# Performance work log

Hardware: AMD Instinct MI355X
Metric: run time of the kernel (lower is better)

The kernel has to match this reference:

```python
import jax, jax.numpy as jnp
import numpy as np

N = 262144   # tokens
L = 128      # ldims (per-direction LSTM feature size)
H = 128      # hidden_units
H2 = 128     # hidden2_units
R = 64       # number of relation labels


def setup_inputs() -> dict:
    key = jax.random.key(0)
    ks = jax.random.split(key, 12)
    glorot = lambda k, shape: jax.random.uniform(
        k, shape, jnp.float32, -1.0, 1.0) * np.sqrt(6.0 / (shape[0] + shape[1]))
    return {
        "fwd": jax.random.normal(ks[0], (N, L), jnp.float32),
        "bwd": jax.random.normal(ks[1], (N, L), jnp.float32),
        "gold_heads": jax.random.randint(ks[2], (N - 1,), 0, N),
        "gold_rels": jax.random.randint(ks[3], (N - 1,), 0, R),
        "WFOH": glorot(ks[4], (2 * L, H)),
        "WFOM": glorot(ks[5], (2 * L, H)),
        "rhidBias": glorot(ks[6], (1, H)),
        "rcatBias": glorot(ks[7], (1, 2 * H)),
        "rhid2Layer": glorot(ks[8], (2 * H, H2)),
        "rhid2Bias": glorot(ks[9], (1, H2)),
        "routLayer": glorot(ks[10], (H2, R)),
        "routBias": glorot(ks[11], (1, R)),
    }


def reference(fwd, bwd, gold_heads, gold_rels, WFOH, WFOM, rhidBias,
              rcatBias, rhid2Layer, rhid2Bias, routLayer, routBias):
    E = gold_heads.shape[0]
    mods = jnp.arange(E) + 1                       # modifiers are tokens 1..N-1
    # per-edge concat(head fwd-state, modifier bwd-state): (E, 2L)
    cat = jnp.concatenate([fwd[gold_heads], bwd[mods]], axis=-1)
    headfov = cat @ WFOH                           # (E, H)
    modfov = cat @ WFOM                            # (E, H)
    # hidden2_units > 0 branch of __evaluateLabel
    h = jnp.tanh(jnp.concatenate([headfov, modfov], axis=-1) + rcatBias)  # (E, 2H)
    h2 = jnp.tanh(h @ rhid2Layer + rhid2Bias)      # (E, H2)
    scores = h2 @ routLayer + routBias             # (E, R)
    # hinge: best wrong label vs gold label, loss only if margin violated
    gold_s = jnp.take_along_axis(scores, gold_rels[:, None], axis=1)[:, 0]
    masked = jnp.where(jnp.arange(R)[None, :] == gold_rels[:, None], -jnp.inf, scores)
    wrong_idx = jnp.argmax(masked, axis=1)
    wrong_s = jnp.take_along_axis(scores, wrong_idx[:, None], axis=1)[:, 0]
    lerrs = jnp.where(gold_s < wrong_s + 1.0, wrong_s - gold_s, 0.0)  # (E,)
    return lerrs
```

## Files before the change

### kernel.cpp

```cpp
#include <hip/hip_runtime.h>
#include <hip/hip_bf16.h>

typedef __bf16 bf16x8 __attribute__((ext_vector_type(8)));
typedef float  f32x4  __attribute__((ext_vector_type(4)));

#define MFMA16 __builtin_amdgcn_mfma_f32_16x16x32_bf16

__device__ __forceinline__ float fast_tanh(float x) {
    float e = __builtin_amdgcn_exp2f(x * 2.8853900817779268f);
    return 1.0f - 2.0f * __builtin_amdgcn_rcpf(e + 1.0f);
}

__device__ __forceinline__ unsigned short f2bf(float f) {
    unsigned u = __builtin_bit_cast(unsigned, f);
    u += 0x7fffu + ((u >> 16) & 1u);
    return (unsigned short)(u >> 16);
}

__global__ __launch_bounds__(512, 2) void rel_kernel(
    const float* __restrict__ fwd, const float* __restrict__ bwd,
    const int* __restrict__ gold_heads, const int* __restrict__ gold_rels,
    const float* __restrict__ WFOH, const float* __restrict__ WFOM,
    const float* __restrict__ rcatBias, const float* __restrict__ rhid2Layer,
    const float* __restrict__ rhid2Bias, const float* __restrict__ routLayer,
    const float* __restrict__ routBias, float* __restrict__ out,
    int E, int NT)
{
    __shared__ __align__(16) char sh_cat[32 * 512];
    __shared__ __align__(16) char sh_h  [32 * 512];
    __shared__ __align__(16) char sh_h2 [32 * 256];
    __shared__ __align__(16) char sh_sc [32 * 256];
    __shared__ float sh_catf[256];
    __shared__ float sh_hf[256];
    __shared__ float sh_h2f[128];
    __shared__ float sh_scf[64];
    __shared__ int sh_nfix;
    __shared__ int sh_fixlist[8];

    const int tid   = threadIdx.x;
    const int w     = tid >> 6;
    const int lane  = tid & 63;
    const int row16 = lane & 15;
    const int g     = lane >> 4;
    const int xm    = (row16 & 7) << 4;

    bf16x8 w1f[2][8];
    #pragma unroll
    for (int nbl = 0; nbl < 2; ++nbl) {
        int n = 32 * w + 16 * nbl + row16;
        const float* Wsrc = (n < 128) ? WFOH : WFOM;
        int col = (n < 128) ? n : (n - 128);
        #pragma unroll
        for (int kk = 0; kk < 8; ++kk) {
            bf16x8 f;
            #pragma unroll
            for (int j = 0; j < 8; ++j) {
                int k = 32 * kk + 8 * g + j;
                f[j] = (__bf16)Wsrc[k * 128 + col];
            }
            w1f[nbl][kk] = f;
        }
    }
    bf16x8 w2f[8];
    {
        int n2 = 16 * w + row16;
        #pragma unroll
        for (int kk = 0; kk < 8; ++kk) {
            bf16x8 f;
            #pragma unroll
            for (int j = 0; j < 8; ++j) {
                int k = 32 * kk + 8 * g + j;
                f[j] = (__bf16)rhid2Layer[k * 128 + n2];
            }
            w2f[kk] = f;
        }
    }
    const int mb3 = w >> 2, nb3 = w & 3;
    bf16x8 w3f[4];
    {
        int n3 = 16 * nb3 + row16;
        #pragma unroll
        for (int kk = 0; kk < 4; ++kk) {
            bf16x8 f;
            #pragma unroll
            for (int j = 0; j < 8; ++j) {
                int k = 32 * kk + 8 * g + j;
                f[j] = (__bf16)routLayer[k * 64 + n3];
            }
            w3f[kk] = f;
        }
    }
    const float rcb0 = rcatBias[32 * w + row16];
    const float rcb1 = rcatBias[32 * w + 16 + row16];
    const float r2b  = rhid2Bias[16 * w + row16];
    const float rob  = routBias[16 * nb3 + row16];

    const int sr = tid >> 4;
    const int sq = tid & 15;
    const int xr_st = (sr & 7) << 4;

    float4 pf[4];
    auto load_tile = [&](int t) {
        int e = t * 32 + sr;
        if (e < E) {
            const float* src;
            if (sq < 8) {
                int head = gold_heads[e];
                src = fwd + (size_t)head * 128 + sq * 16;
            } else {
                src = bwd + (size_t)(e + 1) * 128 + (sq - 8) * 16;
            }
            const float4* p4 = reinterpret_cast<const float4*>(src);
            #pragma unroll
            for (int c = 0; c < 4; ++c) pf[c] = p4[c];
        } else {
            #pragma unroll
            for (int c = 0; c < 4; ++c) pf[c] = make_float4(0.f, 0.f, 0.f, 0.f);
        }
    };

    int tile0 = blockIdx.x;
    if (tile0 < NT) load_tile(tile0);

    for (int tile = tile0; tile < NT; tile += gridDim.x) {
        const int e0 = tile * 32;

        #pragma unroll
        for (int c = 0; c < 4; ++c) {
            uint2 pk;
            pk.x = (unsigned)f2bf(pf[c].x) | ((unsigned)f2bf(pf[c].y) << 16);
            pk.y = (unsigned)f2bf(pf[c].z) | ((unsigned)f2bf(pf[c].w) << 16);
            int off = sr * 512 + ((32 * sq + 8 * c) ^ xr_st);
            *(uint2*)(sh_cat + off) = pk;
        }
        __syncthreads();

        if (tile + gridDim.x < NT) load_tile(tile + gridDim.x);

        f32x4 acc1[2][2];
        #pragma unroll
        for (int a = 0; a < 2; ++a)
            #pragma unroll
            for (int b = 0; b < 2; ++b) acc1[a][b] = (f32x4){0.f, 0.f, 0.f, 0.f};
        #pragma unroll
        for (int kk = 0; kk < 8; ++kk) {
            int ko = (64 * kk + 16 * g) ^ xm;
            bf16x8 a0 = *(const bf16x8*)(sh_cat + row16 * 512 + ko);
            bf16x8 a1 = *(const bf16x8*)(sh_cat + (16 + row16) * 512 + ko);
            acc1[0][0] = MFMA16(a0, w1f[0][kk], acc1[0][0], 0, 0, 0);
            acc1[1][0] = MFMA16(a1, w1f[0][kk], acc1[1][0], 0, 0, 0);
            acc1[0][1] = MFMA16(a0, w1f[1][kk], acc1[0][1], 0, 0, 0);
            acc1[1][1] = MFMA16(a1, w1f[1][kk], acc1[1][1], 0, 0, 0);
        }
        #pragma unroll
        for (int mb = 0; mb < 2; ++mb)
            #pragma unroll
            for (int nbl = 0; nbl < 2; ++nbl) {
                float bias = nbl ? rcb1 : rcb0;
                #pragma unroll
                for (int r = 0; r < 4; ++r) {
                    int row = 16 * mb + 4 * g + r;
                    int col = 32 * w + 16 * nbl + row16;
                    float v = fast_tanh(acc1[mb][nbl][r] + bias);
                    int off = row * 512 + ((2 * col) ^ ((row & 7) << 4));
                    *(unsigned short*)(sh_h + off) = f2bf(v);
                }
            }
        __syncthreads();

        f32x4 acc2[2];
        acc2[0] = (f32x4){0.f, 0.f, 0.f, 0.f};
        acc2[1] = (f32x4){0.f, 0.f, 0.f, 0.f};
        #pragma unroll
        for (int kk = 0; kk < 8; ++kk) {
            int ko = (64 * kk + 16 * g) ^ xm;
            bf16x8 a0 = *(const bf16x8*)(sh_h + row16 * 512 + ko);
            bf16x8 a1 = *(const bf16x8*)(sh_h + (16 + row16) * 512 + ko);
            acc2[0] = MFMA16(a0, w2f[kk], acc2[0], 0, 0, 0);
            acc2[1] = MFMA16(a1, w2f[kk], acc2[1], 0, 0, 0);
        }
        #pragma unroll
        for (int mb = 0; mb < 2; ++mb)
            #pragma unroll
            for (int r = 0; r < 4; ++r) {
                int row = 16 * mb + 4 * g + r;
                int col = 16 * w + row16;
                float v = fast_tanh(acc2[mb][r] + r2b);
                int off = row * 256 + ((2 * col) ^ ((row & 7) << 4));
                *(unsigned short*)(sh_h2 + off) = f2bf(v);
            }
        __syncthreads();

        f32x4 acc3 = (f32x4){0.f, 0.f, 0.f, 0.f};
        #pragma unroll
        for (int kk = 0; kk < 4; ++kk) {
            int m = 16 * mb3 + row16;
            int off = m * 256 + ((64 * kk + 16 * g) ^ xm);
            bf16x8 a = *(const bf16x8*)(sh_h2 + off);
            acc3 = MFMA16(a, w3f[kk], acc3, 0, 0, 0);
        }
        if (tid == 0) sh_nfix = 0;
        #pragma unroll
        for (int r = 0; r < 4; ++r) {
            int row = 16 * mb3 + 4 * g + r;
            int col = 16 * nb3 + row16;
            float v = acc3[r] + rob;
            int off = row * 256 + ((4 * col) ^ ((row & 7) << 4));
            *(float*)(sh_sc + off) = v;
        }
        __syncthreads();

        {
            int r  = tid >> 4;
            int g4 = tid & 15;
            int e  = e0 + r;
            int off = r * 256 + ((16 * g4) ^ ((r & 7) << 4));
            f32x4 sv = *(const f32x4*)(sh_sc + off);
            int gold = (e < E) ? gold_rels[e] : 0;
            float gs = -3.0e38f, ws = -3.0e38f;
            #pragma unroll
            for (int c = 0; c < 4; ++c) {
                int lab = 4 * g4 + c;
                float v = sv[c];
                if (lab == gold) gs = v; else ws = fmaxf(ws, v);
            }
            #pragma unroll
            for (int o = 1; o < 16; o <<= 1) {
                gs = fmaxf(gs, __shfl_xor(gs, o));
                ws = fmaxf(ws, __shfl_xor(ws, o));
            }
            if (g4 == 0 && e < E) {
                out[e] = (gs < ws + 1.0f) ? (ws - gs) : 0.0f;
                if (fabsf((gs - ws) - 1.0f) < 0.125f) {
                    int idx = atomicAdd(&sh_nfix, 1);
                    if (idx < 8) sh_fixlist[idx] = r;
                }
            }
        }
        __syncthreads();

        int nf = sh_nfix;
        nf = nf > 8 ? 8 : nf;
        for (int i = 0; i < nf; ++i) {
            int e = e0 + sh_fixlist[i];
            if (tid < 256) {
                int head = gold_heads[e];
                sh_catf[tid] = (tid < 128) ? fwd[(size_t)head * 128 + tid]
                                           : bwd[(size_t)(e + 1) * 128 + (tid - 128)];
            }
            __syncthreads();
            if (tid < 256) {
                const float* base = (tid < 128) ? WFOH : WFOM;
                int col = (tid < 128) ? tid : tid - 128;
                float s = 0.f;
                #pragma unroll 8
                for (int k = 0; k < 256; ++k) s += sh_catf[k] * base[k * 128 + col];
                sh_hf[tid] = tanhf(s + rcatBias[tid]);
            }
            __syncthreads();
            if (tid < 128) {
                float s = 0.f;
                #pragma unroll 8
                for (int k = 0; k < 256; ++k) s += sh_hf[k] * rhid2Layer[k * 128 + tid];
                sh_h2f[tid] = tanhf(s + rhid2Bias[tid]);
            }
            __syncthreads();
            if (tid < 64) {
                float s = 0.f;
                #pragma unroll 8
                for (int k = 0; k < 128; ++k) s += sh_h2f[k] * routLayer[k * 64 + tid];
                sh_scf[tid] = s + routBias[tid];
            }
            __syncthreads();
            if (tid < 64) {
                int gold = gold_rels[e];
                float v = sh_scf[tid];
                float gs = (tid == gold) ? v : -3.0e38f;
                float ws = (tid == gold) ? -3.0e38f : v;
                #pragma unroll
                for (int o = 1; o < 64; o <<= 1) {
                    gs = fmaxf(gs, __shfl_xor(gs, o));
                    ws = fmaxf(ws, __shfl_xor(ws, o));
                }
                if (tid == 0) out[e] = (gs < ws + 1.0f) ? (ws - gs) : 0.0f;
            }
            __syncthreads();
        }
    }
}

extern "C" void kernel_launch(void* const* d_in, const int* in_sizes, int n_in,
                              void* d_out, int out_size, void* d_ws, size_t ws_size,
                              hipStream_t stream) {
    const float* fwd        = (const float*)d_in[0];
    const float* bwd        = (const float*)d_in[1];
    const int*   gold_heads = (const int*)d_in[2];
    const int*   gold_rels  = (const int*)d_in[3];
    const float* WFOH       = (const float*)d_in[4];
    const float* WFOM       = (const float*)d_in[5];
    const float* rcatBias   = (const float*)d_in[7];
    const float* rhid2      = (const float*)d_in[8];
    const float* rhid2Bias  = (const float*)d_in[9];
    const float* rout       = (const float*)d_in[10];
    const float* routBias   = (const float*)d_in[11];
    float* out = (float*)d_out;

    int E = in_sizes[2];
    if (E <= 0) return;
    int NT = (E + 31) / 32;
    int grid = NT < 512 ? NT : 512;

    hipLaunchKernelGGL(rel_kernel, dim3(grid), dim3(512), 0, stream,
                       fwd, bwd, gold_heads, gold_rels, WFOH, WFOM, rcatBias,
                       rhid2, rhid2Bias, rout, routBias, out, E, NT);
}
```

Before: 193.1 us.

## Enlarge edge tile to 128 rows per block with permuted-K layer weights

Raises the tile from 32 to 128 edges per iteration so each wave issues many more MFMAs per barrier and per weight-register set. Layer-2 and layer-3 weights are loaded with a permuted K index (kinv) so the paired bf16x2 stores of hidden activations match the MFMA operand order, and the conversions use native bf16 casts. Next-tile loads now overlap layers 2–3, and the scalar fallback path splits its reductions across more threads. In exchange, shared memory grows to 128 KB, each thread holds 16 float4 prefetch registers, and the grid shrinks to 256 blocks, which can lower occupancy.

```diff
diff --git a/kernel.cpp b/kernel.cpp
--- a/kernel.cpp
+++ b/kernel.cpp
@@ -2,6 +2,7 @@
 #include <hip/hip_bf16.h>
 
 typedef __bf16 bf16x8 __attribute__((ext_vector_type(8)));
+typedef __bf16 bf16x2 __attribute__((ext_vector_type(2)));
 typedef float  f32x4  __attribute__((ext_vector_type(4)));
 
 #define MFMA16 __builtin_amdgcn_mfma_f32_16x16x32_bf16
@@ -11,10 +12,8 @@
     return 1.0f - 2.0f * __builtin_amdgcn_rcpf(e + 1.0f);
 }
 
-__device__ __forceinline__ unsigned short f2bf(float f) {
-    unsigned u = __builtin_bit_cast(unsigned, f);
-    u += 0x7fffu + ((u >> 16) & 1u);
-    return (unsigned short)(u >> 16);
+__device__ __forceinline__ int kinv(int ke) {
+    return (ke & ~31) | ((ke & 1) << 4) | ((ke >> 1) & 15);
 }
 
 __global__ __launch_bounds__(512, 2) void rel_kernel(
@@ -26,16 +25,16 @@
     const float* __restrict__ routBias, float* __restrict__ out,
     int E, int NT)
 {
-    __shared__ __align__(16) char sh_cat[32 * 512];
-    __shared__ __align__(16) char sh_h  [32 * 512];
-    __shared__ __align__(16) char sh_h2 [32 * 256];
-    __shared__ __align__(16) char sh_sc [32 * 256];
-    __shared__ float sh_catf[256];
-    __shared__ float sh_hf[256];
-    __shared__ float sh_h2f[128];
-    __shared__ float sh_scf[64];
+    __shared__ __align__(16) char smem[131072];
     __shared__ int sh_nfix;
-    __shared__ int sh_fixlist[8];
+    __shared__ int sh_fixlist[16];
+
+    char* const sh_cat = smem;
+    char* const sh_h   = smem + 65536;
+    float* const fx_cat = (float*)(smem + 98304);
+    float* const fx_h   = fx_cat + 256;
+    float* const fx_h2  = fx_h + 256;
+    float* const fx_p   = fx_h2 + 128;
 
     const int tid   = threadIdx.x;
     const int w     = tid >> 6;
@@ -43,238 +42,239 @@
     const int row16 = lane & 15;
     const int g     = lane >> 4;
     const int xm    = (row16 & 7) << 4;
+    const int q4    = w & 3;
+    const int hw    = w >> 2;
 
     bf16x8 w1f[2][8];
     #pragma unroll
     for (int nbl = 0; nbl < 2; ++nbl) {
-        int n = 32 * w + 16 * nbl + row16;
-        const float* Wsrc = (n < 128) ? WFOH : WFOM;
-        int col = (n < 128) ? n : (n - 128);
+        const int n = 32 * w + 16 * nbl + row16;
+        const float* Wsrc = (32 * w + 16 * nbl < 128) ? WFOH : WFOM;
+        const int col = n & 127;
         #pragma unroll
         for (int kk = 0; kk < 8; ++kk) {
             bf16x8 f;
             #pragma unroll
-            for (int j = 0; j < 8; ++j) {
-                int k = 32 * kk + 8 * g + j;
-                f[j] = (__bf16)Wsrc[k * 128 + col];
-            }
+            for (int j = 0; j < 8; ++j) f[j] = (__bf16)Wsrc[(32 * kk + 8 * g + j) * 128 + col];
             w1f[nbl][kk] = f;
         }
     }
-    bf16x8 w2f[8];
-    {
-        int n2 = 16 * w + row16;
+    bf16x8 w2f[2][8];
+    #pragma unroll
+    for (int nbl = 0; nbl < 2; ++nbl) {
+        const int n2 = 32 * q4 + 16 * nbl + row16;
         #pragma unroll
         for (int kk = 0; kk < 8; ++kk) {
             bf16x8 f;
             #pragma unroll
-            for (int j = 0; j < 8; ++j) {
-                int k = 32 * kk + 8 * g + j;
-                f[j] = (__bf16)rhid2Layer[k * 128 + n2];
-            }
-            w2f[kk] = f;
+            for (int j = 0; j < 8; ++j) f[j] = (__bf16)rhid2Layer[kinv(32 * kk + 8 * g + j) * 128 + n2];
+            w2f[nbl][kk] = f;
         }
     }
-    const int mb3 = w >> 2, nb3 = w & 3;
     bf16x8 w3f[4];
     {
-        int n3 = 16 * nb3 + row16;
+        const int n3 = 16 * q4 + row16;
         #pragma unroll
         for (int kk = 0; kk < 4; ++kk) {
             bf16x8 f;
             #pragma unroll
-            for (int j = 0; j < 8; ++j) {
-                int k = 32 * kk + 8 * g + j;
-                f[j] = (__bf16)routLayer[k * 64 + n3];
-            }
+            for (int j = 0; j < 8; ++j) f[j] = (__bf16)routLayer[kinv(32 * kk + 8 * g + j) * 64 + n3];
             w3f[kk] = f;
         }
     }
     const float rcb0 = rcatBias[32 * w + row16];
     const float rcb1 = rcatBias[32 * w + 16 + row16];
-    const float r2b  = rhid2Bias[16 * w + row16];
-    const float rob  = routBias[16 * nb3 + row16];
-
-    const int sr = tid >> 4;
-    const int sq = tid & 15;
-    const int xr_st = (sr & 7) << 4;
-
-    float4 pf[4];
+    const float r2b0 = rhid2Bias[32 * q4 + row16];
+    const float r2b1 = rhid2Bias[32 * q4 + 16 + row16];
+    const float rob  = routBias[16 * q4 + row16];
+
+    const int r_s = tid >> 2;
+    const int q_s = tid & 3;
+    const int xr  = (r_s & 7) << 4;
+
+    float4 pf[16];
     auto load_tile = [&](int t) {
-        int e = t * 32 + sr;
+        const int e = t * 128 + r_s;
         if (e < E) {
             const float* src;
-            if (sq < 8) {
-                int head = gold_heads[e];
-                src = fwd + (size_t)head * 128 + sq * 16;
+            if (q_s < 2) {
+                const int head = gold_heads[e];
+                src = fwd + (size_t)head * 128 + 64 * q_s;
             } else {
-                src = bwd + (size_t)(e + 1) * 128 + (sq - 8) * 16;
+                src = bwd + (size_t)(e + 1) * 128 + 64 * (q_s - 2);
             }
             const float4* p4 = reinterpret_cast<const float4*>(src);
             #pragma unroll
-            for (int c = 0; c < 4; ++c) pf[c] = p4[c];
+            for (int i = 0; i < 16; ++i) pf[i] = p4[i];
         } else {
             #pragma unroll
-            for (int c = 0; c < 4; ++c) pf[c] = make_float4(0.f, 0.f, 0.f, 0.f);
+            for (int i = 0; i < 16; ++i) pf[i] = make_float4(0.f, 0.f, 0.f, 0.f);
         }
     };
 
-    int tile0 = blockIdx.x;
-    if (tile0 < NT) load_tile(tile0);
-
-    for (int tile = tile0; tile < NT; tile += gridDim.x) {
-        const int e0 = tile * 32;
-
-        #pragma unroll
-        for (int c = 0; c < 4; ++c) {
-            uint2 pk;
-            pk.x = (unsigned)f2bf(pf[c].x) | ((unsigned)f2bf(pf[c].y) << 16);
-            pk.y = (unsigned)f2bf(pf[c].z) | ((unsigned)f2bf(pf[c].w) << 16);
-            int off = sr * 512 + ((32 * sq + 8 * c) ^ xr_st);
-            *(uint2*)(sh_cat + off) = pk;
-        }
-        __syncthreads();
-
-        if (tile + gridDim.x < NT) load_tile(tile + gridDim.x);
-
-        f32x4 acc1[2][2];
-        #pragma unroll
-        for (int a = 0; a < 2; ++a)
-            #pragma unroll
-            for (int b = 0; b < 2; ++b) acc1[a][b] = (f32x4){0.f, 0.f, 0.f, 0.f};
+    load_tile(blockIdx.x);
+
+    for (int tile = blockIdx.x; tile < NT; tile += gridDim.x) {
+        const int e0 = tile * 128;
+
+        #pragma unroll
+        for (int i = 0; i < 8; ++i) {
+            bf16x8 v;
+            v[0] = (__bf16)pf[2 * i].x;     v[1] = (__bf16)pf[2 * i].y;
+            v[2] = (__bf16)pf[2 * i].z;     v[3] = (__bf16)pf[2 * i].w;
+            v[4] = (__bf16)pf[2 * i + 1].x; v[5] = (__bf16)pf[2 * i + 1].y;
+            v[6] = (__bf16)pf[2 * i + 1].z; v[7] = (__bf16)pf[2 * i + 1].w;
+            *(bf16x8*)(sh_cat + r_s * 512 + ((128 * q_s + 16 * i) ^ xr)) = v;
+        }
+        __syncthreads();
+
+        f32x4 acc1[8][2];
+        #pragma unroll
+        for (int mb = 0; mb < 8; ++mb) {
+            acc1[mb][0] = (f32x4){0.f, 0.f, 0.f, 0.f};
+            acc1[mb][1] = (f32x4){0.f, 0.f, 0.f, 0.f};
+        }
         #pragma unroll
         for (int kk = 0; kk < 8; ++kk) {
-            int ko = (64 * kk + 16 * g) ^ xm;
-            bf16x8 a0 = *(const bf16x8*)(sh_cat + row16 * 512 + ko);
-            bf16x8 a1 = *(const bf16x8*)(sh_cat + (16 + row16) * 512 + ko);
-            acc1[0][0] = MFMA16(a0, w1f[0][kk], acc1[0][0], 0, 0, 0);
-            acc1[1][0] = MFMA16(a1, w1f[0][kk], acc1[1][0], 0, 0, 0);
-            acc1[0][1] = MFMA16(a0, w1f[1][kk], acc1[0][1], 0, 0, 0);
-            acc1[1][1] = MFMA16(a1, w1f[1][kk], acc1[1][1], 0, 0, 0);
-        }
-        #pragma unroll
-        for (int mb = 0; mb < 2; ++mb)
-            #pragma unroll
-            for (int nbl = 0; nbl < 2; ++nbl) {
-                float bias = nbl ? rcb1 : rcb0;
+            const int ko = (64 * kk + 16 * g) ^ xm;
+            #pragma unroll
+            for (int mb = 0; mb < 8; ++mb) {
+                const bf16x8 a = *(const bf16x8*)(sh_cat + (16 * mb + row16) * 512 + ko);
+                acc1[mb][0] = MFMA16(a, w1f[0][kk], acc1[mb][0], 0, 0, 0);
+                acc1[mb][1] = MFMA16(a, w1f[1][kk], acc1[mb][1], 0, 0, 0);
+            }
+        }
+        #pragma unroll
+        for (int mb = 0; mb < 8; ++mb) {
+            #pragma unroll
+            for (int r = 0; r < 4; ++r) {
+                const int row = 16 * mb + 4 * g + r;
+                bf16x2 p;
+                p[0] = (__bf16)fast_tanh(acc1[mb][0][r] + rcb0);
+                p[1] = (__bf16)fast_tanh(acc1[mb][1][r] + rcb1);
+                *(bf16x2*)(sh_h + row * 512 + ((64 * w + 4 * row16) ^ ((row & 7) << 4))) = p;
+            }
+        }
+        __syncthreads();
+
+        f32x4 acc2[4][2];
+        #pragma unroll
+        for (int i = 0; i < 4; ++i) {
+            acc2[i][0] = (f32x4){0.f, 0.f, 0.f, 0.f};
+            acc2[i][1] = (f32x4){0.f, 0.f, 0.f, 0.f};
+        }
+        #pragma unroll
+        for (int kk = 0; kk < 8; ++kk) {
+            const int ko = (64 * kk + 16 * g) ^ xm;
+            #pragma unroll
+            for (int i = 0; i < 4; ++i) {
+                const bf16x8 a = *(const bf16x8*)(sh_h + (16 * (4 * hw + i) + row16) * 512 + ko);
+                acc2[i][0] = MFMA16(a, w2f[0][kk], acc2[i][0], 0, 0, 0);
+                acc2[i][1] = MFMA16(a, w2f[1][kk], acc2[i][1], 0, 0, 0);
+            }
+        }
+        if (tile + (int)gridDim.x < NT) load_tile(tile + gridDim.x);
+        #pragma unroll
+        for (int i = 0; i < 4; ++i) {
+            #pragma unroll
+            for (int r = 0; r < 4; ++r) {
+                const int row = 16 * (4 * hw + i) + 4 * g + r;
+                bf16x2 p;
+                p[0] = (__bf16)fast_tanh(acc2[i][0][r] + r2b0);
+                p[1] = (__bf16)fast_tanh(acc2[i][1][r] + r2b1);
+                *(bf16x2*)(sh_cat + row * 256 + ((64 * q4 + 4 * row16) ^ ((row & 7) << 4))) = p;
+            }
+        }
+        __syncthreads();
+
+        f32x4 acc3[4];
+        #pragma unroll
+        for (int i = 0; i < 4; ++i) acc3[i] = (f32x4){0.f, 0.f, 0.f, 0.f};
+        if (tid == 0) sh_nfix = 0;
+        #pragma unroll
+        for (int kk = 0; kk < 4; ++kk) {
+            const int ko = (64 * kk + 16 * g) ^ xm;
+            #pragma unroll
+            for (int i = 0; i < 4; ++i) {
+                const bf16x8 a = *(const bf16x8*)(sh_cat + (16 * (4 * hw + i) + row16) * 256 + ko);
+                acc3[i] = MFMA16(a, w3f[kk], acc3[i], 0, 0, 0);
+            }
+        }
+        #pragma unroll
+        for (int i = 0; i < 4; ++i) {
+            #pragma unroll
+            for (int r = 0; r < 4; ++r) {
+                const int row = 16 * (4 * hw + i) + 4 * g + r;
+                *(float*)(sh_h + row * 256 + ((64 * q4 + 4 * row16) ^ ((row & 7) << 4))) = acc3[i][r] + rob;
+            }
+        }
+        __syncthreads();
+
+        {
+            const int r = tid >> 2, q = tid & 3;
+            const int e = e0 + r;
+            const int gold = (e < E) ? gold_rels[e] : 0;
+            float gs = -3.0e38f, ws = -3.0e38f;
+            #pragma unroll
+            for (int c = 0; c < 4; ++c) {
+                const f32x4 sv = *(const f32x4*)(sh_h + r * 256 + ((64 * q + 16 * c) ^ ((r & 7) << 4)));
                 #pragma unroll
-                for (int r = 0; r < 4; ++r) {
-                    int row = 16 * mb + 4 * g + r;
-                    int col = 32 * w + 16 * nbl + row16;
-                    float v = fast_tanh(acc1[mb][nbl][r] + bias);
-                    int off = row * 512 + ((2 * col) ^ ((row & 7) << 4));
-                    *(unsigned short*)(sh_h + off) = f2bf(v);
+                for (int cc = 0; cc < 4; ++cc) {
+                    const int lab = 16 * q + 4 * c + cc;
+                    const float v = sv[cc];
+                    if (lab == gold) gs = v; else ws = fmaxf(ws, v);
                 }
             }
-        __syncthreads();
-
-        f32x4 acc2[2];
-        acc2[0] = (f32x4){0.f, 0.f, 0.f, 0.f};
-        acc2[1] = (f32x4){0.f, 0.f, 0.f, 0.f};
-        #pragma unroll
-        for (int kk = 0; kk < 8; ++kk) {
-            int ko = (64 * kk + 16 * g) ^ xm;
-            bf16x8 a0 = *(const bf16x8*)(sh_h + row16 * 512 + ko);
-            bf16x8 a1 = *(const bf16x8*)(sh_h + (16 + row16) * 512 + ko);
-            acc2[0] = MFMA16(a0, w2f[kk], acc2[0], 0, 0, 0);
-            acc2[1] = MFMA16(a1, w2f[kk], acc2[1], 0, 0, 0);
-        }
-        #pragma unroll
-        for (int mb = 0; mb < 2; ++mb)
-            #pragma unroll
-            for (int r = 0; r < 4; ++r) {
-                int row = 16 * mb + 4 * g + r;
-                int col = 16 * w + row16;
-                float v = fast_tanh(acc2[mb][r] + r2b);
-                int off = row * 256 + ((2 * col) ^ ((row & 7) << 4));
-                *(unsigned short*)(sh_h2 + off) = f2bf(v);
-            }
-        __syncthreads();
-
-        f32x4 acc3 = (f32x4){0.f, 0.f, 0.f, 0.f};
-        #pragma unroll
-        for (int kk = 0; kk < 4; ++kk) {
-            int m = 16 * mb3 + row16;
-            int off = m * 256 + ((64 * kk + 16 * g) ^ xm);
-            bf16x8 a = *(const bf16x8*)(sh_h2 + off);
-            acc3 = MFMA16(a, w3f[kk], acc3, 0, 0, 0);
-        }
-        if (tid == 0) sh_nfix = 0;
-        #pragma unroll
-        for (int r = 0; r < 4; ++r) {
-            int row = 16 * mb3 + 4 * g + r;
-            int col = 16 * nb3 + row16;
-            float v = acc3[r] + rob;
-            int off = row * 256 + ((4 * col) ^ ((row & 7) << 4));
-            *(float*)(sh_sc + off) = v;
-        }
-        __syncthreads();
-
-        {
-            int r  = tid >> 4;
-            int g4 = tid & 15;
-            int e  = e0 + r;
-            int off = r * 256 + ((16 * g4) ^ ((r & 7) << 4));
-            f32x4 sv = *(const f32x4*)(sh_sc + off);
-            int gold = (e < E) ? gold_rels[e] : 0;
-            float gs = -3.0e38f, ws = -3.0e38f;
-            #pragma unroll
-            for (int c = 0; c < 4; ++c) {
-                int lab = 4 * g4 + c;
-                float v = sv[c];
-                if (lab == gold) gs = v; else ws = fmaxf(ws, v);
-            }
-            #pragma unroll
-            for (int o = 1; o < 16; o <<= 1) {
-                gs = fmaxf(gs, __shfl_xor(gs, o));
-                ws = fmaxf(ws, __shfl_xor(ws, o));
-            }
-            if (g4 == 0 && e < E) {
+            gs = fmaxf(gs, __shfl_xor(gs, 1)); ws = fmaxf(ws, __shfl_xor(ws, 1));
+            gs = fmaxf(gs, __shfl_xor(gs, 2)); ws = fmaxf(ws, __shfl_xor(ws, 2));
+            if (q == 0 && e < E) {
                 out[e] = (gs < ws + 1.0f) ? (ws - gs) : 0.0f;
                 if (fabsf((gs - ws) - 1.0f) < 0.125f) {
-                    int idx = atomicAdd(&sh_nfix, 1);
-                    if (idx < 8) sh_fixlist[idx] = r;
+                    const int idx = atomicAdd(&sh_nfix, 1);
+                    if (idx < 16) sh_fixlist[idx] = r;
                 }
             }
         }
         __syncthreads();
 
-        int nf = sh_nfix;
-        nf = nf > 8 ? 8 : nf;
-        for (int i = 0; i < nf; ++i) {
-            int e = e0 + sh_fixlist[i];
+        int nf = sh_nfix; if (nf > 16) nf = 16;
+        for (int fi = 0; fi < nf; ++fi) {
+            const int e = e0 + sh_fixlist[fi];
+            __syncthreads();
             if (tid < 256) {
-                int head = gold_heads[e];
-                sh_catf[tid] = (tid < 128) ? fwd[(size_t)head * 128 + tid]
-                                           : bwd[(size_t)(e + 1) * 128 + (tid - 128)];
-            }
-            __syncthreads();
-            if (tid < 256) {
-                const float* base = (tid < 128) ? WFOH : WFOM;
-                int col = (tid < 128) ? tid : tid - 128;
+                const int head = gold_heads[e];
+                fx_cat[tid] = (tid < 128) ? fwd[(size_t)head * 128 + tid]
+                                          : bwd[(size_t)(e + 1) * 128 + (tid - 128)];
+            }
+            __syncthreads();
+            {
+                const int d = tid & 255, half = tid >> 8;
+                const float* base = (d < 128) ? WFOH : WFOM;
+                const int col = d & 127;
                 float s = 0.f;
                 #pragma unroll 8
-                for (int k = 0; k < 256; ++k) s += sh_catf[k] * base[k * 128 + col];
-                sh_hf[tid] = tanhf(s + rcatBias[tid]);
-            }
-            __syncthreads();
-            if (tid < 128) {
+                for (int k = 128 * half; k < 128 * half + 128; ++k) s += fx_cat[k] * base[k * 128 + col];
+                fx_p[half * 256 + d] = s;
+            }
+            __syncthreads();
+            if (tid < 256) fx_h[tid] = tanhf(fx_p[tid] + fx_p[256 + tid] + rcatBias[tid]);
+            __syncthreads();
+            {
+                const int d2 = tid & 127, qq = tid >> 7;
                 float s = 0.f;
                 #pragma unroll 8
-                for (int k = 0; k < 256; ++k) s += sh_hf[k] * rhid2Layer[k * 128 + tid];
-                sh_h2f[tid] = tanhf(s + rhid2Bias[tid]);
-            }
+                for (int k = 64 * qq; k < 64 * qq + 64; ++k) s += fx_h[k] * rhid2Layer[k * 128 + d2];
+                fx_p[qq * 128 + d2] = s;
+            }
+            __syncthreads();
+            if (tid < 128) fx_h2[tid] = tanhf(fx_p[tid] + fx_p[128 + tid] + fx_p[256 + tid] + fx_p[384 + tid] + rhid2Bias[tid]);
             __syncthreads();
             if (tid < 64) {
                 float s = 0.f;
                 #pragma unroll 8
-                for (int k = 0; k < 128; ++k) s += sh_h2f[k] * routLayer[k * 64 + tid];
-                sh_scf[tid] = s + routBias[tid];
-            }
-            __syncthreads();
-            if (tid < 64) {
-                int gold = gold_rels[e];
-                float v = sh_scf[tid];
+                for (int k = 0; k < 128; ++k) s += fx_h2[k] * routLayer[k * 64 + tid];
+                const float v = s + routBias[tid];
+                const int gold = gold_rels[e];
                 float gs = (tid == gold) ? v : -3.0e38f;
                 float ws = (tid == gold) ? -3.0e38f : v;
                 #pragma unroll
@@ -284,7 +284,6 @@
                 }
                 if (tid == 0) out[e] = (gs < ws + 1.0f) ? (ws - gs) : 0.0f;
             }
-            __syncthreads();
         }
     }
 }
@@ -305,10 +304,10 @@
     const float* routBias   = (const float*)d_in[11];
     float* out = (float*)d_out;
 
-    int E = in_sizes[2];
+    const int E = in_sizes[2];
     if (E <= 0) return;
-    int NT = (E + 31) / 32;
-    int grid = NT < 512 ? NT : 512;
+    const int NT = (E + 127) / 128;
+    const int grid = NT < 256 ? NT : 256;
 
     hipLaunchKernelGGL(rel_kernel, dim3(grid), dim3(512), 0, stream,
                        fwd, bwd, gold_heads, gold_rels, WFOH, WFOM, rcatBias,
```

Result: slower. 500.7 us (+159.3%).
